# Kernel optimization log

Measured on AMD Instinct MI355X. Metric: run time of the kernel, lower is better.

Reference implementation:

```python
import jax, jax.numpy as jnp
import numpy as np

B, N, E = 2, 10000, 160000
D, DC, L = 512, 8, 3
EPS = 1e-5


def layer_norm(x, g, b):
    m = jnp.mean(x, axis=-1, keepdims=True)
    v = jnp.mean((x - m) ** 2, axis=-1, keepdims=True)
    return (x - m) * jax.lax.rsqrt(v + EPS) * g + b


def setup_inputs() -> dict:
    key = jax.random.key(0)
    ks = jax.random.split(key, 8)
    node_features = jax.random.normal(ks[0], (B, N, D), dtype=jnp.float32)
    edge_index = jax.random.randint(ks[1], (2, E), 0, N, dtype=jnp.int64)
    edge_attr = jax.random.normal(ks[2], (E, D), dtype=jnp.float32)
    # manifold coordinate projection
    W_coord = jax.random.normal(ks[3], (D, DC), dtype=jnp.float32) / np.sqrt(D)
    # per-layer causal field layers (modeled as linear) and layer norms
    W_field = jax.random.normal(ks[4], (L, D, D), dtype=jnp.float32) / np.sqrt(D)
    b_field = jnp.zeros((L, D), dtype=jnp.float32)
    ln_g = jnp.ones((L, D), dtype=jnp.float32)
    ln_b = jnp.zeros((L, D), dtype=jnp.float32)
    # output projection: LayerNorm + Linear
    out_ln_g = jnp.ones((D,), dtype=jnp.float32)
    out_ln_b = jnp.zeros((D,), dtype=jnp.float32)
    W_out = jax.random.normal(ks[5], (D, D), dtype=jnp.float32) / np.sqrt(D)
    b_out = jnp.zeros((D,), dtype=jnp.float32)
    return dict(node_features=node_features, edge_index=edge_index, edge_attr=edge_attr,
                W_coord=W_coord, W_field=W_field, b_field=b_field, ln_g=ln_g, ln_b=ln_b,
                out_ln_g=out_ln_g, out_ln_b=out_ln_b, W_out=W_out, b_out=b_out)


def reference(node_features, edge_index, edge_attr, W_coord, W_field, b_field,
              ln_g, ln_b, out_ln_g, out_ln_b, W_out, b_out):
    src, dst = edge_index[0], edge_index[1]
    # node coordinates from manifold projection (computed once, from inputs)
    coords = node_features @ W_coord                        # (B, N, DC)
    # transport factor per edge, per batch: exp(-||dst_coord - src_coord||)
    coord_diff = coords[:, dst] - coords[:, src]            # (B, E, DC)
    transport = jnp.exp(-jnp.linalg.norm(coord_diff, axis=-1, keepdims=True))  # (B, E, 1)
    # degree of destination nodes (same for every batch element)
    deg = jnp.zeros((N,), dtype=node_features.dtype).at[dst].add(1.0)
    deg = jnp.clip(deg, 1.0, None)[None, :, None]           # (1, N, 1)

    x = node_features
    edge_msg = None
    for l in range(L):
        x_field = x @ W_field[l] + b_field[l]               # (B, N, D)
        # gather src features, apply transport, add edge attributes
        edge_msg = x_field[:, src] * transport + edge_attr[None]  # (B, E, D)
        # scatter-add into destination nodes, normalize by degree
        upd = jnp.zeros_like(x).at[:, dst].add(edge_msg)    # (B, N, D)
        x = layer_norm(x + upd / deg, ln_g[l], ln_b[l])
    node_output = layer_norm(x, out_ln_g, out_ln_b) @ W_out + b_out
    return node_output, edge_msg
```

## Files before the change

### kernel.cpp

```cpp
#include <hip/hip_runtime.h>
#include <stdint.h>

#define NN 10000
#define EE 160000
#define BB 2
#define DD 512
#define KC 1024
#define MVALID 20000
#define MPAD 20096
#define LEPS 1e-5f

typedef __bf16 bf16_t;
typedef __bf16 bf16x8 __attribute__((ext_vector_type(8)));
typedef float f32x4 __attribute__((ext_vector_type(4)));
typedef float f32x2 __attribute__((ext_vector_type(2)));

__device__ inline void gload16(const void* g, void* l) {
  __builtin_amdgcn_global_load_lds((const __attribute__((address_space(1))) uint32_t*)g,
                                   (__attribute__((address_space(3))) uint32_t*)l,
                                   16, 0, 0);
}

__global__ __launch_bounds__(256) void convw_k(const float* __restrict__ Wf,
                                               const float* __restrict__ Wo,
                                               const float* __restrict__ olng,
                                               bf16_t* __restrict__ wcat) {
  __shared__ float tile[64][65];
  const int kt = blockIdx.x, nt = blockIdx.y, l = blockIdx.z;
  const float* W = (l < 3) ? (Wf + (size_t)l * 262144) : Wo;
  const int tn = threadIdx.x & 63;
  const int tk = threadIdx.x >> 6;
#pragma unroll
  for (int i = 0; i < 16; i++) {
    const int kl = tk + i * 4;
    tile[kl][tn] = W[(size_t)(kt * 64 + kl) * 512 + nt * 64 + tn];
  }
  __syncthreads();
  const int kl2 = threadIdx.x & 63;
  const int nb = threadIdx.x >> 6;
  const float gk = (l == 3) ? olng[kt * 64 + kl2] : 1.0f;
#pragma unroll
  for (int i = 0; i < 16; i++) {
    const int nl = nb + i * 4;
    bf16_t h = (bf16_t)(tile[kl2][nl] * gk);
    wcat[((size_t)l * 512 + nt * 64 + nl) * 512 + kt * 64 + kl2] = h;
  }
}

__global__ __launch_bounds__(512) void ubinit_k(const float* __restrict__ bo, float* __restrict__ ub) {
  ub[threadIdx.x] = bo[threadIdx.x];
}
__global__ __launch_bounds__(256) void ubacc_k(const float* __restrict__ olnb,
                                               const float* __restrict__ Wo,
                                               float* __restrict__ ub) {
  const int k0 = blockIdx.x * 16;
  const int tid = threadIdx.x;
#pragma unroll
  for (int h = 0; h < 2; h++) {
    const int n = tid + h * 256;
    float s = 0.f;
#pragma unroll
    for (int kk = 0; kk < 16; kk++) s += olnb[k0 + kk] * Wo[(size_t)(k0 + kk) * 512 + n];
    atomicAdd(&ub[n], s);
  }
}

__global__ __launch_bounds__(256) void coords_k(const float* __restrict__ x,
                                                const float* __restrict__ Wc,
                                                float* __restrict__ out,
                                                bf16_t* __restrict__ xcat) {
  __shared__ float smW[DD * 8];
  for (int i = threadIdx.x; i < DD * 8; i += 256) smW[i] = Wc[i];
  __syncthreads();
  const int wave = threadIdx.x >> 6, lane = threadIdx.x & 63;
  const int n = blockIdx.x * 4 + wave;
  const int b = blockIdx.y;
  const size_t row = (size_t)b * NN + n;
  const float* xr = x + row * DD + lane * 8;
  f32x4 x0 = *(const f32x4*)xr;
  f32x4 x1 = *(const f32x4*)(xr + 4);
  bf16x8 hi, lo;
#pragma unroll
  for (int j = 0; j < 8; j++) {
    float v = (j < 4) ? x0[j] : x1[j - 4];
    bf16_t h = (bf16_t)v;
    hi[j] = h;
    lo[j] = (bf16_t)(v - (float)h);
  }
  bf16_t* xc = xcat + row * KC + lane * 8;
  *(bf16x8*)xc = hi;
  *(bf16x8*)(xc + DD) = lo;
  float a[8];
#pragma unroll
  for (int dc = 0; dc < 8; dc++) a[dc] = 0.f;
#pragma unroll
  for (int j = 0; j < 8; j++) {
    float xv = (j < 4) ? x0[j] : x1[j - 4];
    const float* wrow = smW + (lane * 8 + j) * 8;
#pragma unroll
    for (int dc = 0; dc < 8; dc++) a[dc] += xv * wrow[dc];
  }
#pragma unroll
  for (int dc = 0; dc < 8; dc++)
    for (int o = 32; o >= 1; o >>= 1) a[dc] += __shfl_xor(a[dc], o);
  if (lane == 0) {
#pragma unroll
    for (int dc = 0; dc < 8; dc++) out[row * 8 + dc] = a[dc];
  }
}

__global__ __launch_bounds__(256) void transport_deg_k(const float* __restrict__ coords,
                                                       const int* __restrict__ srcA,
                                                       const int* __restrict__ dstA,
                                                       float* __restrict__ tr,
                                                       int* __restrict__ degc) {
  int e = blockIdx.x * 256 + threadIdx.x;
  int s = srcA[e], d = dstA[e];
#pragma unroll
  for (int b = 0; b < BB; b++) {
    const float* cs = coords + ((size_t)b * NN + s) * 8;
    const float* cd = coords + ((size_t)b * NN + d) * 8;
    float ss = 0.f;
#pragma unroll
    for (int i = 0; i < 8; i++) {
      float df = cd[i] - cs[i];
      ss += df * df;
    }
    tr[(size_t)b * EE + e] = expf(-sqrtf(ss));
  }
  atomicAdd(&degc[d], 1);
}

__global__ __launch_bounds__(1024) void scan_k(const int* __restrict__ cnt, int* __restrict__ rowptr,
                                               float* __restrict__ invdeg) {
  __shared__ int part[1024];
  const int tid = threadIdx.x;
  const int CH = 10;
  int base = tid * CH;
  int local[CH];
  int s = 0;
#pragma unroll
  for (int i = 0; i < CH; i++) {
    int n = base + i;
    int c = (n < NN) ? cnt[n] : 0;
    local[i] = s;
    s += c;
  }
  part[tid] = s;
  __syncthreads();
  for (int off = 1; off < 1024; off <<= 1) {
    int v = (tid >= off) ? part[tid - off] : 0;
    __syncthreads();
    part[tid] += v;
    __syncthreads();
  }
  int excl = (tid > 0) ? part[tid - 1] : 0;
#pragma unroll
  for (int i = 0; i < CH; i++) {
    int n = base + i;
    if (n < NN) {
      rowptr[n] = excl + local[i];
      int c = cnt[n];
      invdeg[n] = 1.0f / (float)(c > 1 ? c : 1);
    }
  }
  if (tid == 0) rowptr[NN] = EE;
}

__global__ __launch_bounds__(256) void fill_k(const int* __restrict__ dstA, const int* __restrict__ rowptr,
                                              int* __restrict__ fill, int* __restrict__ eidA) {
  int e = blockIdx.x * 256 + threadIdx.x;
  int d = dstA[e];
  int pos = rowptr[d] + atomicAdd(&fill[d], 1);
  eidA[pos] = e;
}

__global__ __launch_bounds__(256) void remap_k(const int* __restrict__ eidA,
                                               const int* __restrict__ srcA,
                                               const int* __restrict__ dstA,
                                               const float* __restrict__ tr,
                                               const float* __restrict__ invdeg,
                                               int* __restrict__ srcs,
                                               float* __restrict__ trs) {
  int i = blockIdx.x * 256 + threadIdx.x;
  const int e = eidA[i];
  const int s = srcA[e];
  const float idg = invdeg[dstA[e]];
  srcs[i] = s;
  trs[i] = tr[e] * idg;
  trs[(size_t)EE + i] = tr[(size_t)EE + e] * idg;
}

__global__ __launch_bounds__(256) void gemm_bt_b(const bf16_t* __restrict__ A,
                                                 const bf16_t* __restrict__ Bw,
                                                 const float* __restrict__ bias,
                                                 bf16_t* __restrict__ C, int mvalid) {
  __shared__ __align__(16) char smem[16384];
  const int tid = threadIdx.x;
  const int lane = tid & 63;
  const int wave = tid >> 6;
  const int mtile = blockIdx.x;
  const int ntile = blockIdx.y;
  const int wr = wave >> 1, wc = wave & 1;
  const int r = tid >> 2;
  const int c = tid & 3;
  const size_t aRow0 = (size_t)(mtile * 128 + r);
  const size_t bRow0 = (size_t)(ntile * 128 + r);
  char* smA = smem;
  char* smB = smem + 8192;
  char* ldsA0 = smA + tid * 16;
  char* ldsA1 = smA + 4096 + tid * 16;
  char* ldsB0 = smB + tid * 16;
  char* ldsB1 = smB + 4096 + tid * 16;

  f32x4 acc[4][4];
#pragma unroll
  for (int m = 0; m < 4; m++)
#pragma unroll
    for (int n = 0; n < 4; n++) acc[m][n] = (f32x4){0.f, 0.f, 0.f, 0.f};

  const int koff = (lane >> 4) * 16;
  const int arow = wr * 64 + (lane & 15);
  const int brow = wc * 64 + (lane & 15);

  for (int kk = 0; kk < 16; ++kk) {
    const int kbase = kk * 32 + c * 8;
    gload16(A + aRow0 * KC + kbase, ldsA0);
    gload16(A + (aRow0 + 64) * KC + kbase, ldsA1);
    gload16(Bw + bRow0 * 512 + kbase, ldsB0);
    gload16(Bw + (bRow0 + 64) * 512 + kbase, ldsB1);
    __syncthreads();
    bf16x8 af[4], bfr[4];
#pragma unroll
    for (int m = 0; m < 4; m++) af[m] = *(const bf16x8*)(smA + (arow + m * 16) * 64 + koff);
#pragma unroll
    for (int n = 0; n < 4; n++) bfr[n] = *(const bf16x8*)(smB + (brow + n * 16) * 64 + koff);
#pragma unroll
    for (int m = 0; m < 4; m++)
#pragma unroll
      for (int n = 0; n < 4; n++)
        acc[m][n] = __builtin_amdgcn_mfma_f32_16x16x32_bf16(af[m], bfr[n], acc[m][n], 0, 0, 0);
    __syncthreads();
  }

  const int crow0 = mtile * 128 + wr * 64 + (lane >> 4) * 4;
  const int ccol0 = ntile * 128 + wc * 64 + (lane & 15);
#pragma unroll
  for (int n = 0; n < 4; n++) {
    const int col = ccol0 + n * 16;
    const float bv = bias[col];
#pragma unroll
    for (int m = 0; m < 4; m++) {
      const int rw = crow0 + m * 16;
#pragma unroll
      for (int j = 0; j < 4; j++) {
        int rowi = rw + j;
        if (rowi < mvalid) C[(size_t)rowi * DD + col] = (bf16_t)(acc[m][n][j] + bv);
      }
    }
  }
}

__global__ __launch_bounds__(256) void gemm_bt_f(const bf16_t* __restrict__ A,
                                                 const bf16_t* __restrict__ Bw,
                                                 const float* __restrict__ bias,
                                                 float* __restrict__ C, int mvalid,
                                                 const float* __restrict__ rs) {
  __shared__ __align__(16) char smem[16384];
  const int tid = threadIdx.x;
  const int lane = tid & 63;
  const int wave = tid >> 6;
  const int mtile = blockIdx.x;
  const int ntile = blockIdx.y;
  const int wr = wave >> 1, wc = wave & 1;
  const int r = tid >> 2;
  const int c = tid & 3;
  const size_t aRow0 = (size_t)(mtile * 128 + r);
  const size_t bRow0 = (size_t)(ntile * 128 + r);
  char* smA = smem;
  char* smB = smem + 8192;
  char* ldsA0 = smA + tid * 16;
  char* ldsA1 = smA + 4096 + tid * 16;
  char* ldsB0 = smB + tid * 16;
  char* ldsB1 = smB + 4096 + tid * 16;

  f32x4 acc[4][4];
#pragma unroll
  for (int m = 0; m < 4; m++)
#pragma unroll
    for (int n = 0; n < 4; n++) acc[m][n] = (f32x4){0.f, 0.f, 0.f, 0.f};

  const int koff = (lane >> 4) * 16;
  const int arow = wr * 64 + (lane & 15);
  const int brow = wc * 64 + (lane & 15);

  for (int kk = 0; kk < 16; ++kk) {
    const int kbase = kk * 32 + c * 8;
    gload16(A + aRow0 * KC + kbase, ldsA0);
    gload16(A + (aRow0 + 64) * KC + kbase, ldsA1);
    gload16(Bw + bRow0 * 512 + kbase, ldsB0);
    gload16(Bw + (bRow0 + 64) * 512 + kbase, ldsB1);
    __syncthreads();
    bf16x8 af[4], bfr[4];
#pragma unroll
    for (int m = 0; m < 4; m++) af[m] = *(const bf16x8*)(smA + (arow + m * 16) * 64 + koff);
#pragma unroll
    for (int n = 0; n < 4; n++) bfr[n] = *(const bf16x8*)(smB + (brow + n * 16) * 64 + koff);
#pragma unroll
    for (int m = 0; m < 4; m++)
#pragma unroll
      for (int n = 0; n < 4; n++)
        acc[m][n] = __builtin_amdgcn_mfma_f32_16x16x32_bf16(af[m], bfr[n], acc[m][n], 0, 0, 0);
    __syncthreads();
  }

  const int crow0 = mtile * 128 + wr * 64 + (lane >> 4) * 4;
  const int ccol0 = ntile * 128 + wc * 64 + (lane & 15);
#pragma unroll
  for (int n = 0; n < 4; n++) {
    const int col = ccol0 + n * 16;
    const float bv = bias[col];
#pragma unroll
    for (int m = 0; m < 4; m++) {
      const int rw = crow0 + m * 16;
#pragma unroll
      for (int j = 0; j < 4; j++) {
        int rowi = rw + j;
        if (rowi < mvalid) C[(size_t)rowi * DD + col] = acc[m][n][j] * rs[rowi] + bv;
      }
    }
  }
}

template <int FUSE_EA>
__global__ __launch_bounds__(256) void layer_k(const bf16_t* __restrict__ xfield,
                                               const float* __restrict__ nf, int is_l0, int outstat,
                                               bf16_t* __restrict__ xcat,
                                               const int* __restrict__ srcs,
                                               const float* __restrict__ trs,
                                               const int* __restrict__ rowptr,
                                               const int* __restrict__ eidA,
                                               const float* __restrict__ eattr,
                                               const float* __restrict__ invdeg,
                                               float* __restrict__ eagg,
                                               const float* __restrict__ g,
                                               const float* __restrict__ bbias,
                                               float* __restrict__ rs_out) {
  const int wave = threadIdx.x >> 6, lane = threadIdx.x & 63;
  const int n = blockIdx.x * 4 + wave;
  const int d0 = lane * 8;
  const int beg = rowptr[n], end = rowptr[n + 1];
  const bf16_t* xf0 = xfield + (size_t)0 * NN * DD + d0;
  const bf16_t* xf1 = xfield + (size_t)1 * NN * DD + d0;
  const float* trs1p = trs + EE;
  float acc0[8], acc1[8], eac[8];
#pragma unroll
  for (int j = 0; j < 8; j++) acc0[j] = acc1[j] = eac[j] = 0.f;

  for (int c0 = beg; c0 < end; c0 += 64) {
    const int cnt = min(64, end - c0);
    int s_r = 0, e_r = 0;
    float t0_r = 0.f, t1_r = 0.f;
    if (lane < cnt) {
      s_r = srcs[c0 + lane];
      t0_r = trs[c0 + lane];
      t1_r = trs1p[c0 + lane];
      if (FUSE_EA) e_r = eidA[c0 + lane];
    }
    for (int j = 0; j < cnt; j += 4) {
#pragma unroll
      for (int u = 0; u < 4; u++) {
        const int jj = j + u;
        const int s = __shfl(s_r, jj);
        const float t0 = __shfl(t0_r, jj);
        const float t1 = __shfl(t1_r, jj);
        const bf16x8 xv0 = *(const bf16x8*)(xf0 + (size_t)s * DD);
        const bf16x8 xv1 = *(const bf16x8*)(xf1 + (size_t)s * DD);
        if (FUSE_EA) {
          const int e = __shfl(e_r, jj);
          const bool act = jj < cnt;
          const f32x4 r0 = __builtin_nontemporal_load((const f32x4*)(eattr + (size_t)e * DD + d0));
          const f32x4 r1 = __builtin_nontemporal_load((const f32x4*)(eattr + (size_t)e * DD + d0 + 4));
          if (act) {
#pragma unroll
            for (int q = 0; q < 8; q++) eac[q] += (q < 4) ? r0[q & 3] : r1[q & 3];
          }
        }
#pragma unroll
        for (int q = 0; q < 8; q++) {
          acc0[q] += t0 * (float)xv0[q];
          acc1[q] += t1 * (float)xv1[q];
        }
      }
    }
  }

  float ea8[8];
  if (FUSE_EA) {
    const float idg = invdeg[n];
#pragma unroll
    for (int j = 0; j < 8; j++) ea8[j] = eac[j] * idg;
    f32x4 o0, o1;
#pragma unroll
    for (int j = 0; j < 4; j++) {
      o0[j] = ea8[j];
      o1[j] = ea8[j + 4];
    }
    *(f32x4*)(eagg + (size_t)n * DD + d0) = o0;
    *(f32x4*)(eagg + (size_t)n * DD + d0 + 4) = o1;
  } else {
    const f32x4 e0 = *(const f32x4*)(eagg + (size_t)n * DD + d0);
    const f32x4 e1 = *(const f32x4*)(eagg + (size_t)n * DD + d0 + 4);
#pragma unroll
    for (int j = 0; j < 8; j++) ea8[j] = (j < 4) ? e0[j] : e1[j - 4];
  }

  bf16_t* xc0 = xcat + (size_t)n * KC + d0;
  bf16_t* xc1 = xcat + (size_t)(NN + n) * KC + d0;
  float xp0[8], xp1[8];
  if (is_l0) {
    const f32x4 p00 = *(const f32x4*)(nf + (size_t)n * DD + d0);
    const f32x4 p01 = *(const f32x4*)(nf + (size_t)n * DD + d0 + 4);
    const f32x4 p10 = *(const f32x4*)(nf + (size_t)(NN + n) * DD + d0);
    const f32x4 p11 = *(const f32x4*)(nf + (size_t)(NN + n) * DD + d0 + 4);
#pragma unroll
    for (int j = 0; j < 8; j++) {
      xp0[j] = (j < 4) ? p00[j] : p01[j - 4];
      xp1[j] = (j < 4) ? p10[j] : p11[j - 4];
    }
  } else {
    const bf16x8 h0 = *(const bf16x8*)(xc0);
    const bf16x8 l0v = *(const bf16x8*)(xc0 + DD);
    const bf16x8 h1 = *(const bf16x8*)(xc1);
    const bf16x8 l1v = *(const bf16x8*)(xc1 + DD);
#pragma unroll
    for (int j = 0; j < 8; j++) {
      xp0[j] = (float)h0[j] + (float)l0v[j];
      xp1[j] = (float)h1[j] + (float)l1v[j];
    }
  }
  float v0[8], v1[8];
  float s10 = 0.f, s20 = 0.f, s11 = 0.f, s21 = 0.f;
#pragma unroll
  for (int j = 0; j < 8; j++) {
    v0[j] = xp0[j] + acc0[j] + ea8[j];
    v1[j] = xp1[j] + acc1[j] + ea8[j];
    s10 += v0[j];
    s20 += v0[j] * v0[j];
    s11 += v1[j];
    s21 += v1[j] * v1[j];
  }
#pragma unroll
  for (int o = 32; o >= 1; o >>= 1) {
    s10 += __shfl_xor(s10, o);
    s20 += __shfl_xor(s20, o);
    s11 += __shfl_xor(s11, o);
    s21 += __shfl_xor(s21, o);
  }
  const float mean0 = s10 * (1.f / 512.f);
  const float rs0 = rsqrtf(s20 * (1.f / 512.f) - mean0 * mean0 + LEPS);
  const float mean1 = s11 * (1.f / 512.f);
  const float rs1 = rsqrtf(s21 * (1.f / 512.f) - mean1 * mean1 + LEPS);
  const f32x4 g0 = *(const f32x4*)(g + d0);
  const f32x4 g1 = *(const f32x4*)(g + d0 + 4);
  const f32x4 b0 = *(const f32x4*)(bbias + d0);
  const f32x4 b1 = *(const f32x4*)(bbias + d0 + 4);
  float y0[8], y1[8];
  float sy10 = 0.f, sy20 = 0.f, sy11 = 0.f, sy21 = 0.f;
#pragma unroll
  for (int j = 0; j < 8; j++) {
    const float gg = (j < 4) ? g0[j] : g1[j - 4];
    const float bb = (j < 4) ? b0[j] : b1[j - 4];
    y0[j] = (v0[j] - mean0) * rs0 * gg + bb;
    y1[j] = (v1[j] - mean1) * rs1 * gg + bb;
    sy10 += y0[j];
    sy20 += y0[j] * y0[j];
    sy11 += y1[j];
    sy21 += y1[j] * y1[j];
  }
  float sub0 = 0.f, sub1 = 0.f;
  if (outstat) {
#pragma unroll
    for (int o = 32; o >= 1; o >>= 1) {
      sy10 += __shfl_xor(sy10, o);
      sy20 += __shfl_xor(sy20, o);
      sy11 += __shfl_xor(sy11, o);
      sy21 += __shfl_xor(sy21, o);
    }
    const float my0 = sy10 * (1.f / 512.f);
    const float rsy0 = rsqrtf(sy20 * (1.f / 512.f) - my0 * my0 + LEPS);
    const float my1 = sy11 * (1.f / 512.f);
    const float rsy1 = rsqrtf(sy21 * (1.f / 512.f) - my1 * my1 + LEPS);
    if (lane == 0) {
      rs_out[n] = rsy0;
      rs_out[NN + n] = rsy1;
    }
    sub0 = my0;
    sub1 = my1;
  }
  bf16x8 ho0, lo0, ho1, lo1;
#pragma unroll
  for (int j = 0; j < 8; j++) {
    const float ya = y0[j] - sub0;
    const float yb = y1[j] - sub1;
    bf16_t ha = (bf16_t)ya;
    bf16_t hb = (bf16_t)yb;
    ho0[j] = ha;
    lo0[j] = (bf16_t)(ya - (float)ha);
    ho1[j] = hb;
    lo1[j] = (bf16_t)(yb - (float)hb);
  }
  *(bf16x8*)xc0 = ho0;
  *(bf16x8*)(xc0 + DD) = lo0;
  *(bf16x8*)xc1 = ho1;
  *(bf16x8*)(xc1 + DD) = lo1;
}

__global__ __launch_bounds__(256) void edgemsg_k(const bf16_t* __restrict__ xfield,
                                                 const float* __restrict__ transport,
                                                 const int* __restrict__ srcA,
                                                 const float* __restrict__ eattr,
                                                 float* __restrict__ out) {
  const int wv = threadIdx.x >> 6, lane = threadIdx.x & 63;
  const int e = blockIdx.x * 4 + wv;
  const int d0 = lane * 8;
  const int s = srcA[e];
  const f32x4 a0 = __builtin_nontemporal_load((const f32x4*)(eattr + (size_t)e * DD + d0));
  const f32x4 a1 = __builtin_nontemporal_load((const f32x4*)(eattr + (size_t)e * DD + d0 + 4));
  const float t0 = transport[e];
  const float t1 = transport[(size_t)EE + e];
  const bf16x8 x0 = *(const bf16x8*)(xfield + (size_t)s * DD + d0);
  const bf16x8 x1 = *(const bf16x8*)(xfield + ((size_t)NN + s) * DD + d0);
  f32x4 o00, o01, o10, o11;
#pragma unroll
  for (int j = 0; j < 4; j++) {
    o00[j] = (float)x0[j] * t0 + a0[j];
    o01[j] = (float)x0[j + 4] * t0 + a1[j];
    o10[j] = (float)x1[j] * t1 + a0[j];
    o11[j] = (float)x1[j + 4] * t1 + a1[j];
  }
  float* ob0 = out + (size_t)e * DD + d0;
  float* ob1 = out + ((size_t)EE + e) * DD + d0;
  __builtin_nontemporal_store(o00, (f32x4*)ob0);
  __builtin_nontemporal_store(o01, (f32x4*)(ob0 + 4));
  __builtin_nontemporal_store(o10, (f32x4*)ob1);
  __builtin_nontemporal_store(o11, (f32x4*)(ob1 + 4));
}

extern "C" void kernel_launch(void* const* d_in, const int* in_sizes, int n_in,
                              void* d_out, int out_size, void* d_ws, size_t ws_size,
                              hipStream_t stream) {
  const float* nf = (const float*)d_in[0];
  const int* eidx = (const int*)d_in[1];
  const float* eattr = (const float*)d_in[2];
  const float* Wc = (const float*)d_in[3];
  const float* Wf = (const float*)d_in[4];
  const float* bfield = (const float*)d_in[5];
  const float* lng = (const float*)d_in[6];
  const float* lnb = (const float*)d_in[7];
  const float* olng = (const float*)d_in[8];
  const float* olnb = (const float*)d_in[9];
  const float* Wo = (const float*)d_in[10];
  const float* bo = (const float*)d_in[11];
  const int* srcA = eidx;
  const int* dstA = eidx + EE;
  float* outp = (float*)d_out;

  char* ws = (char*)d_ws;
  size_t off = 0;
  auto alloc = [&](size_t bytes) {
    void* p = ws + off;
    off += (bytes + 255) & ~(size_t)255;
    return p;
  };
  bf16_t* xcat = (bf16_t*)alloc((size_t)MPAD * KC * 2);
  bf16_t* xfield = (bf16_t*)alloc((size_t)MPAD * DD * 2);
  bf16_t* wcat = (bf16_t*)alloc((size_t)4 * DD * 512 * 2);
  float* eagg = (float*)alloc((size_t)NN * DD * 4);
  float* coords = (float*)alloc((size_t)BB * NN * 8 * 4);
  float* transport = (float*)alloc((size_t)BB * EE * 4);
  float* trs = (float*)alloc((size_t)BB * EE * 4);
  int* srcs = (int*)alloc(EE * 4);
  int* degfill = (int*)alloc((size_t)2 * NN * 4);
  int* degc = degfill;
  int* fillb = degfill + NN;
  int* rowptr = (int*)alloc((NN + 1) * 4);
  int* eidl = (int*)alloc(EE * 4);
  float* invdeg = (float*)alloc(NN * 4);
  float* rs_out = (float*)alloc((size_t)BB * NN * 4);
  float* ub = (float*)alloc(DD * 4);

  hipMemsetAsync(degfill, 0, (size_t)2 * NN * 4, stream);
  hipMemsetAsync(xcat + (size_t)MVALID * KC, 0, (size_t)(MPAD - MVALID) * KC * 2, stream);

  convw_k<<<dim3(8, 8, 4), 256, 0, stream>>>(Wf, Wo, olng, wcat);
  ubinit_k<<<1, 512, 0, stream>>>(bo, ub);
  ubacc_k<<<32, 256, 0, stream>>>(olnb, Wo, ub);
  coords_k<<<dim3(2500, 2), 256, 0, stream>>>(nf, Wc, coords, xcat);
  transport_deg_k<<<625, 256, 0, stream>>>(coords, srcA, dstA, transport, degc);
  scan_k<<<1, 1024, 0, stream>>>(degc, rowptr, invdeg);
  fill_k<<<625, 256, 0, stream>>>(dstA, rowptr, fillb, eidl);
  remap_k<<<625, 256, 0, stream>>>(eidl, srcA, dstA, transport, invdeg, srcs, trs);

  for (int l = 0; l < 3; l++) {
    gemm_bt_b<<<dim3(157, 4), 256, 0, stream>>>(xcat, wcat + (size_t)l * DD * 512,
                                                bfield + l * DD, xfield, MVALID);
    if (l == 2)
      edgemsg_k<<<40000, 256, 0, stream>>>(xfield, transport, srcA, eattr,
                                           outp + (size_t)BB * NN * DD);
    if (l == 0)
      layer_k<1><<<2500, 256, 0, stream>>>(xfield, nf, 1, 0, xcat, srcs, trs, rowptr, eidl, eattr,
                                           invdeg, eagg, lng + l * DD, lnb + l * DD, rs_out);
    else
      layer_k<0><<<2500, 256, 0, stream>>>(xfield, nf, 0, (l == 2) ? 1 : 0, xcat, srcs, trs,
                                           rowptr, eidl, eattr, invdeg, eagg, lng + l * DD,
                                           lnb + l * DD, rs_out);
  }
  gemm_bt_f<<<dim3(157, 4), 256, 0, stream>>>(xcat, wcat + (size_t)3 * DD * 512, ub, outp, MVALID,
                                              rs_out);
}
```

Measured before the change: 651.9 us.

## Fuse final edge-message output into last layer's CSR gather kernel

Removes the standalone edgemsg_k launch and writes the final-layer edge messages from inside the last layer_k pass. That pass already gathers each source row of xfield in destination order, so the separate re-gather of xfield goes away. The cost is an extra read of edge_attr in permuted order and scattered writes to the edge output, using a new raw transport array built in remap_k. It also skips writing the low-precision residual half of xcat in the last layer, on the assumption that the final GEMM does not read it. If gemm_bt_f does use the lo part, that would be a correctness risk.

```diff
diff --git a/kernel.cpp b/kernel.cpp
--- a/kernel.cpp
+++ b/kernel.cpp
@@ -181,14 +181,19 @@
                                                const float* __restrict__ tr,
                                                const float* __restrict__ invdeg,
                                                int* __restrict__ srcs,
-                                               float* __restrict__ trs) {
+                                               float* __restrict__ trs,
+                                               float* __restrict__ trsraw) {
   int i = blockIdx.x * 256 + threadIdx.x;
   const int e = eidA[i];
   const int s = srcA[e];
   const float idg = invdeg[dstA[e]];
+  const float t0 = tr[e];
+  const float t1 = tr[(size_t)EE + e];
   srcs[i] = s;
-  trs[i] = tr[e] * idg;
-  trs[(size_t)EE + i] = tr[(size_t)EE + e] * idg;
+  trs[i] = t0 * idg;
+  trs[(size_t)EE + i] = t1 * idg;
+  trsraw[i] = t0;
+  trsraw[(size_t)EE + i] = t1;
 }
 
 __global__ __launch_bounds__(256) void gemm_bt_b(const bf16_t* __restrict__ A,
@@ -332,17 +337,19 @@
   }
 }
 
-template <int FUSE_EA>
+template <int FUSE_EA, int WRITE_EDGE>
 __global__ __launch_bounds__(256) void layer_k(const bf16_t* __restrict__ xfield,
                                                const float* __restrict__ nf, int is_l0, int outstat,
                                                bf16_t* __restrict__ xcat,
                                                const int* __restrict__ srcs,
                                                const float* __restrict__ trs,
+                                               const float* __restrict__ trsraw,
                                                const int* __restrict__ rowptr,
                                                const int* __restrict__ eidA,
                                                const float* __restrict__ eattr,
                                                const float* __restrict__ invdeg,
                                                float* __restrict__ eagg,
+                                               float* __restrict__ outE,
                                                const float* __restrict__ g,
                                                const float* __restrict__ bbias,
                                                float* __restrict__ rs_out) {
@@ -360,12 +367,16 @@
   for (int c0 = beg; c0 < end; c0 += 64) {
     const int cnt = min(64, end - c0);
     int s_r = 0, e_r = 0;
-    float t0_r = 0.f, t1_r = 0.f;
+    float t0_r = 0.f, t1_r = 0.f, tw0_r = 0.f, tw1_r = 0.f;
     if (lane < cnt) {
       s_r = srcs[c0 + lane];
       t0_r = trs[c0 + lane];
       t1_r = trs1p[c0 + lane];
-      if (FUSE_EA) e_r = eidA[c0 + lane];
+      if (FUSE_EA || WRITE_EDGE) e_r = eidA[c0 + lane];
+      if (WRITE_EDGE) {
+        tw0_r = trsraw[c0 + lane];
+        tw1_r = trsraw[(size_t)EE + c0 + lane];
+      }
     }
     for (int j = 0; j < cnt; j += 4) {
 #pragma unroll
@@ -386,6 +397,29 @@
             for (int q = 0; q < 8; q++) eac[q] += (q < 4) ? r0[q & 3] : r1[q & 3];
           }
         }
+        if (WRITE_EDGE) {
+          const int e = __shfl(e_r, jj);
+          const float tw0 = __shfl(tw0_r, jj);
+          const float tw1 = __shfl(tw1_r, jj);
+          const f32x4 a0 = __builtin_nontemporal_load((const f32x4*)(eattr + (size_t)e * DD + d0));
+          const f32x4 a1 = __builtin_nontemporal_load((const f32x4*)(eattr + (size_t)e * DD + d0 + 4));
+          if (jj < cnt) {
+            f32x4 o00, o01, o10, o11;
+#pragma unroll
+            for (int q = 0; q < 4; q++) {
+              o00[q] = (float)xv0[q] * tw0 + a0[q];
+              o01[q] = (float)xv0[q + 4] * tw0 + a1[q];
+              o10[q] = (float)xv1[q] * tw1 + a0[q];
+              o11[q] = (float)xv1[q + 4] * tw1 + a1[q];
+            }
+            float* ob0 = outE + (size_t)e * DD + d0;
+            float* ob1 = outE + ((size_t)EE + e) * DD + d0;
+            __builtin_nontemporal_store(o00, (f32x4*)ob0);
+            __builtin_nontemporal_store(o01, (f32x4*)(ob0 + 4));
+            __builtin_nontemporal_store(o10, (f32x4*)ob1);
+            __builtin_nontemporal_store(o11, (f32x4*)(ob1 + 4));
+          }
+        }
 #pragma unroll
         for (int q = 0; q < 8; q++) {
           acc0[q] += t0 * (float)xv0[q];
@@ -511,40 +545,11 @@
     lo1[j] = (bf16_t)(yb - (float)hb);
   }
   *(bf16x8*)xc0 = ho0;
-  *(bf16x8*)(xc0 + DD) = lo0;
   *(bf16x8*)xc1 = ho1;
-  *(bf16x8*)(xc1 + DD) = lo1;
-}
-
-__global__ __launch_bounds__(256) void edgemsg_k(const bf16_t* __restrict__ xfield,
-                                                 const float* __restrict__ transport,
-                                                 const int* __restrict__ srcA,
-                                                 const float* __restrict__ eattr,
-                                                 float* __restrict__ out) {
-  const int wv = threadIdx.x >> 6, lane = threadIdx.x & 63;
-  const int e = blockIdx.x * 4 + wv;
-  const int d0 = lane * 8;
-  const int s = srcA[e];
-  const f32x4 a0 = __builtin_nontemporal_load((const f32x4*)(eattr + (size_t)e * DD + d0));
-  const f32x4 a1 = __builtin_nontemporal_load((const f32x4*)(eattr + (size_t)e * DD + d0 + 4));
-  const float t0 = transport[e];
-  const float t1 = transport[(size_t)EE + e];
-  const bf16x8 x0 = *(const bf16x8*)(xfield + (size_t)s * DD + d0);
-  const bf16x8 x1 = *(const bf16x8*)(xfield + ((size_t)NN + s) * DD + d0);
-  f32x4 o00, o01, o10, o11;
-#pragma unroll
-  for (int j = 0; j < 4; j++) {
-    o00[j] = (float)x0[j] * t0 + a0[j];
-    o01[j] = (float)x0[j + 4] * t0 + a1[j];
-    o10[j] = (float)x1[j] * t1 + a0[j];
-    o11[j] = (float)x1[j + 4] * t1 + a1[j];
-  }
-  float* ob0 = out + (size_t)e * DD + d0;
-  float* ob1 = out + ((size_t)EE + e) * DD + d0;
-  __builtin_nontemporal_store(o00, (f32x4*)ob0);
-  __builtin_nontemporal_store(o01, (f32x4*)(ob0 + 4));
-  __builtin_nontemporal_store(o10, (f32x4*)ob1);
-  __builtin_nontemporal_store(o11, (f32x4*)(ob1 + 4));
+  if (!outstat) {
+    *(bf16x8*)(xc0 + DD) = lo0;
+    *(bf16x8*)(xc1 + DD) = lo1;
+  }
 }
 
 extern "C" void kernel_launch(void* const* d_in, const int* in_sizes, int n_in,
@@ -580,6 +585,7 @@
   float* coords = (float*)alloc((size_t)BB * NN * 8 * 4);
   float* transport = (float*)alloc((size_t)BB * EE * 4);
   float* trs = (float*)alloc((size_t)BB * EE * 4);
+  float* trsraw = (float*)alloc((size_t)BB * EE * 4);
   int* srcs = (int*)alloc(EE * 4);
   int* degfill = (int*)alloc((size_t)2 * NN * 4);
   int* degc = degfill;
@@ -600,21 +606,24 @@
   transport_deg_k<<<625, 256, 0, stream>>>(coords, srcA, dstA, transport, degc);
   scan_k<<<1, 1024, 0, stream>>>(degc, rowptr, invdeg);
   fill_k<<<625, 256, 0, stream>>>(dstA, rowptr, fillb, eidl);
-  remap_k<<<625, 256, 0, stream>>>(eidl, srcA, dstA, transport, invdeg, srcs, trs);
-
+  remap_k<<<625, 256, 0, stream>>>(eidl, srcA, dstA, transport, invdeg, srcs, trs, trsraw);
+
+  float* outE = outp + (size_t)BB * NN * DD;
   for (int l = 0; l < 3; l++) {
     gemm_bt_b<<<dim3(157, 4), 256, 0, stream>>>(xcat, wcat + (size_t)l * DD * 512,
                                                 bfield + l * DD, xfield, MVALID);
-    if (l == 2)
-      edgemsg_k<<<40000, 256, 0, stream>>>(xfield, transport, srcA, eattr,
-                                           outp + (size_t)BB * NN * DD);
     if (l == 0)
-      layer_k<1><<<2500, 256, 0, stream>>>(xfield, nf, 1, 0, xcat, srcs, trs, rowptr, eidl, eattr,
-                                           invdeg, eagg, lng + l * DD, lnb + l * DD, rs_out);
+      layer_k<1, 0><<<2500, 256, 0, stream>>>(xfield, nf, 1, 0, xcat, srcs, trs, trsraw, rowptr,
+                                              eidl, eattr, invdeg, eagg, outE, lng + l * DD,
+                                              lnb + l * DD, rs_out);
+    else if (l == 1)
+      layer_k<0, 0><<<2500, 256, 0, stream>>>(xfield, nf, 0, 0, xcat, srcs, trs, trsraw, rowptr,
+                                              eidl, eattr, invdeg, eagg, outE, lng + l * DD,
+                                              lnb + l * DD, rs_out);
     else
-      layer_k<0><<<2500, 256, 0, stream>>>(xfield, nf, 0, (l == 2) ? 1 : 0, xcat, srcs, trs,
-                                           rowptr, eidl, eattr, invdeg, eagg, lng + l * DD,
-                                           lnb + l * DD, rs_out);
+      layer_k<0, 1><<<2500, 256, 0, stream>>>(xfield, nf, 0, 1, xcat, srcs, trs, trsraw, rowptr,
+                                              eidl, eattr, invdeg, eagg, outE, lng + l * DD,
+                                              lnb + l * DD, rs_out);
   }
   gemm_bt_f<<<dim3(157, 4), 256, 0, stream>>>(xcat, wcat + (size_t)3 * DD * 512, ub, outp, MVALID,
                                               rs_out);
```

Result: no change. 663.1 us (+1.7%).
